# Performance work log

Measured on AMD Instinct MI355X. Metric: run time of the kernel, lower is better.

## Reference

```python
import jax, jax.numpy as jnp
import numpy as np

N, M, P = 4096, 4096, 32


def setup_inputs() -> dict:
    key = jax.random.key(0)
    k1, k2 = jax.random.split(key)
    x1 = jax.random.normal(k1, (N, P), dtype=jnp.float32)
    x2 = jax.random.normal(k2, (M, P), dtype=jnp.float32)
    log_rho = jnp.zeros((), dtype=jnp.float32)    # log(1.0)
    log_sigma = jnp.zeros((), dtype=jnp.float32)  # log(1.0)
    return {"x1": x1, "x2": x2, "log_rho": log_rho, "log_sigma": log_sigma}


def reference(x1, x2, log_rho, log_sigma):
    # sigma = exp(log_sigma)^2, rho = exp(log_rho), as in the module's __call__
    sigma = jnp.square(jnp.exp(log_sigma))
    rho = jnp.exp(log_rho)
    xs = x1 / rho  # (n, p)
    ys = x2 / rho  # (m, p)
    # avoids the (n, m, p) broadcasted intermediate of the naive form
    xn = jnp.sum(jnp.square(xs), axis=-1)  # (n,)
    yn = jnp.sum(jnp.square(ys), axis=-1)  # (m,)
    d = xn[:, None] + yn[None, :] - 2.0 * jnp.einsum("np,mp->nm", xs, ys)
    d = jnp.maximum(d, 0.0)  # clamp tiny negative rounding
    K = sigma * jnp.exp(-0.5 * d)  # (n, m)
    return K
```

## Files before the change

### kernel.cpp

```cpp
#include <hip/hip_runtime.h>

#define NN 4096
#define MM 4096
#define PP 32
#define LDA 40

typedef short bf16x8 __attribute__((ext_vector_type(8)));
typedef float f32x4  __attribute__((ext_vector_type(4)));

__device__ __forceinline__ unsigned short f32_to_bf16_rtn(float f) {
    unsigned u = __float_as_uint(f);
    u += 0x7FFF + ((u >> 16) & 1);
    return (unsigned short)(u >> 16);
}

__launch_bounds__(256, 4)
__global__ void eq_fused_mfma_kernel(const float* __restrict__ x1,
                                     const float* __restrict__ x2,
                                     const float* __restrict__ log_rho,
                                     const float* __restrict__ log_sigma,
                                     float* __restrict__ out) {
    __shared__ unsigned short Ah[128 * LDA];
    __shared__ unsigned short Al[128 * LDA];
    __shared__ unsigned short Bh[128 * LDA];
    __shared__ unsigned short Bl[128 * LDA];

    const int t  = threadIdx.x;
    const int bx = blockIdx.x;
    const int by = blockIdx.y;

    {
        const int row  = t >> 1;
        const int half = t & 1;
        {
            const float* src = x1 + (size_t)(by * 128 + row) * PP + half * 16;
            float partial = 0.f;
#pragma unroll
            for (int g = 0; g < 2; ++g) {
                float4 a = *reinterpret_cast<const float4*>(src + g * 8);
                float4 b = *reinterpret_cast<const float4*>(src + g * 8 + 4);
                float vs[8] = {a.x, a.y, a.z, a.w, b.x, b.y, b.z, b.w};
                bf16x8 hv, lv;
#pragma unroll
                for (int e = 0; e < 8; ++e) {
                    float v = vs[e];
                    partial = fmaf(v, v, partial);
                    unsigned short h = f32_to_bf16_rtn(v);
                    hv[e] = (short)h;
                    lv[e] = (short)f32_to_bf16_rtn(v - __uint_as_float((unsigned)h << 16));
                }
                int off = row * LDA + half * 16 + g * 8;
                *reinterpret_cast<bf16x8*>(&Ah[off]) = hv;
                *reinterpret_cast<bf16x8*>(&Al[off]) = lv;
            }
            float full = partial + __shfl_xor(partial, 1);
            if (half == 0) *reinterpret_cast<float*>(&Ah[row * LDA + 32]) = full;
        }
        {
            const float* src = x2 + (size_t)(bx * 128 + row) * PP + half * 16;
            float partial = 0.f;
#pragma unroll
            for (int g = 0; g < 2; ++g) {
                float4 a = *reinterpret_cast<const float4*>(src + g * 8);
                float4 b = *reinterpret_cast<const float4*>(src + g * 8 + 4);
                float vs[8] = {a.x, a.y, a.z, a.w, b.x, b.y, b.z, b.w};
                bf16x8 hv, lv;
#pragma unroll
                for (int e = 0; e < 8; ++e) {
                    float v = vs[e];
                    partial = fmaf(v, v, partial);
                    unsigned short h = f32_to_bf16_rtn(v);
                    hv[e] = (short)h;
                    lv[e] = (short)f32_to_bf16_rtn(v - __uint_as_float((unsigned)h << 16));
                }
                int off = row * LDA + half * 16 + g * 8;
                *reinterpret_cast<bf16x8*>(&Bh[off]) = hv;
                *reinterpret_cast<bf16x8*>(&Bl[off]) = lv;
            }
            float full = partial + __shfl_xor(partial, 1);
            if (half == 0) *reinterpret_cast<float*>(&Bh[row * LDA + 32]) = full;
        }
    }

    const float inv_rho2 = __expf(-2.f * log_rho[0]);
    const float sigma    = __expf(2.f * log_sigma[0]);
    const float nh_ir2   = -0.5f * inv_rho2;

    __syncthreads();

    const int w    = t >> 6;
    const int l    = t & 63;
    const int lo16 = l & 15;
    const int kg   = l >> 4;

    bf16x8 ah[2], al[2];
    float xh[2];
#pragma unroll
    for (int s = 0; s < 2; ++s) {
        int r   = w * 32 + s * 16 + lo16;
        int off = r * LDA + kg * 8;
        ah[s] = *reinterpret_cast<const bf16x8*>(&Ah[off]);
        al[s] = *reinterpret_cast<const bf16x8*>(&Al[off]);
        xh[s] = nh_ir2 * *reinterpret_cast<const float*>(&Ah[r * LDA + 32]);
    }

    const int rbase = by * 128 + w * 32;
    const int cb0   = bx * 128;

#pragma unroll
    for (int ct = 0; ct < 8; ++ct) {
        int off = (ct * 16 + lo16) * LDA + kg * 8;
        bf16x8 bh = *reinterpret_cast<const bf16x8*>(&Bh[off]);
        bf16x8 bl = *reinterpret_cast<const bf16x8*>(&Bl[off]);
        float yh[4];
#pragma unroll
        for (int j = 0; j < 4; ++j)
            yh[j] = nh_ir2 * *reinterpret_cast<const float*>(&Bh[(ct * 16 + kg * 4 + j) * LDA + 32]);
        const int colbase = cb0 + ct * 16 + kg * 4;
#pragma unroll
        for (int s = 0; s < 2; ++s) {
            f32x4 acc = {0.f, 0.f, 0.f, 0.f};
            acc = __builtin_amdgcn_mfma_f32_16x16x32_bf16(bh, ah[s], acc, 0, 0, 0);
            acc = __builtin_amdgcn_mfma_f32_16x16x32_bf16(bh, al[s], acc, 0, 0, 0);
            acc = __builtin_amdgcn_mfma_f32_16x16x32_bf16(bl, ah[s], acc, 0, 0, 0);
            f32x4 K;
            float u0 = fminf(fmaf(inv_rho2, acc[0], xh[s] + yh[0]), 0.f);
            float u1 = fminf(fmaf(inv_rho2, acc[1], xh[s] + yh[1]), 0.f);
            float u2 = fminf(fmaf(inv_rho2, acc[2], xh[s] + yh[2]), 0.f);
            float u3 = fminf(fmaf(inv_rho2, acc[3], xh[s] + yh[3]), 0.f);
            K[0] = sigma * __expf(u0);
            K[1] = sigma * __expf(u1);
            K[2] = sigma * __expf(u2);
            K[3] = sigma * __expf(u3);
            const int row = rbase + s * 16 + lo16;
            *reinterpret_cast<f32x4*>(&out[(size_t)row * MM + colbase]) = K;
        }
    }
}

extern "C" void kernel_launch(void* const* d_in, const int* in_sizes, int n_in,
                              void* d_out, int out_size, void* d_ws, size_t ws_size,
                              hipStream_t stream) {
    const float* x1        = (const float*)d_in[0];
    const float* x2        = (const float*)d_in[1];
    const float* log_rho   = (const float*)d_in[2];
    const float* log_sigma = (const float*)d_in[3];
    float* out = (float*)d_out;

    dim3 grid(MM / 128, NN / 128);
    eq_fused_mfma_kernel<<<grid, 256, 0, stream>>>(x1, x2, log_rho, log_sigma, out);
}
```

Before: 19.60 us.

## Split B tile staging across barrier and fold sigma into exp2 argument

The x2 tile is now loaded into registers up front. Only the first 64 rows are written to LDS before the barrier; the remaining rows are written after it, and a second barrier separates the first four column tiles from the last four, so the early output stores overlap with finishing the B staging. The sigma multiply and exp are replaced by a single exp2 whose argument carries log2e and 2·log_sigma, with the clamp moved to ls2. This adds a second block-wide barrier and changes the numerical form of the exponent.

New measurement: 19.51 us. About the same (-0.4%).

```diff
diff --git a/kernel.cpp b/kernel.cpp
--- a/kernel.cpp
+++ b/kernel.cpp
@@ -7,6 +7,8 @@
 
 typedef short bf16x8 __attribute__((ext_vector_type(8)));
 typedef float f32x4  __attribute__((ext_vector_type(4)));
+
+#define LOG2E 1.44269504088896f
 
 __device__ __forceinline__ unsigned short f32_to_bf16_rtn(float f) {
     unsigned u = __float_as_uint(f);
@@ -29,64 +31,89 @@
     const int bx = blockIdx.x;
     const int by = blockIdx.y;
 
+    const int row  = t >> 1;
+    const int half = t & 1;
+
+    const float* srcB = x2 + (size_t)(bx * 128 + row) * PP + half * 16;
+    float4 bg[4];
+    bg[0] = *reinterpret_cast<const float4*>(srcB + 0);
+    bg[1] = *reinterpret_cast<const float4*>(srcB + 4);
+    bg[2] = *reinterpret_cast<const float4*>(srcB + 8);
+    bg[3] = *reinterpret_cast<const float4*>(srcB + 12);
+
     {
-        const int row  = t >> 1;
-        const int half = t & 1;
-        {
-            const float* src = x1 + (size_t)(by * 128 + row) * PP + half * 16;
-            float partial = 0.f;
+        const float* src = x1 + (size_t)(by * 128 + row) * PP + half * 16;
+        float partial = 0.f;
 #pragma unroll
-            for (int g = 0; g < 2; ++g) {
-                float4 a = *reinterpret_cast<const float4*>(src + g * 8);
-                float4 b = *reinterpret_cast<const float4*>(src + g * 8 + 4);
-                float vs[8] = {a.x, a.y, a.z, a.w, b.x, b.y, b.z, b.w};
-                bf16x8 hv, lv;
+        for (int g = 0; g < 2; ++g) {
+            float4 a = *reinterpret_cast<const float4*>(src + g * 8);
+            float4 b = *reinterpret_cast<const float4*>(src + g * 8 + 4);
+            float vs[8] = {a.x, a.y, a.z, a.w, b.x, b.y, b.z, b.w};
+            bf16x8 hv, lv;
 #pragma unroll
-                for (int e = 0; e < 8; ++e) {
-                    float v = vs[e];
-                    partial = fmaf(v, v, partial);
-                    unsigned short h = f32_to_bf16_rtn(v);
-                    hv[e] = (short)h;
-                    lv[e] = (short)f32_to_bf16_rtn(v - __uint_as_float((unsigned)h << 16));
-                }
-                int off = row * LDA + half * 16 + g * 8;
-                *reinterpret_cast<bf16x8*>(&Ah[off]) = hv;
-                *reinterpret_cast<bf16x8*>(&Al[off]) = lv;
+            for (int e = 0; e < 8; ++e) {
+                float v = vs[e];
+                partial = fmaf(v, v, partial);
+                unsigned short h = f32_to_bf16_rtn(v);
+                hv[e] = (short)h;
+                lv[e] = (short)f32_to_bf16_rtn(v - __uint_as_float((unsigned)h << 16));
             }
-            float full = partial + __shfl_xor(partial, 1);
-            if (half == 0) *reinterpret_cast<float*>(&Ah[row * LDA + 32]) = full;
+            int off = row * LDA + half * 16 + g * 8;
+            *reinterpret_cast<bf16x8*>(&Ah[off]) = hv;
+            *reinterpret_cast<bf16x8*>(&Al[off]) = lv;
         }
-        {
-            const float* src = x2 + (size_t)(bx * 128 + row) * PP + half * 16;
-            float partial = 0.f;
+        float full = partial + __shfl_xor(partial, 1);
+        if (half == 0) *reinterpret_cast<float*>(&Ah[row * LDA + 32]) = full;
+    }
+
+    bf16x8 bhv[2], blv[2];
+    float bfull;
+    {
+        float partial = 0.f;
 #pragma unroll
-            for (int g = 0; g < 2; ++g) {
-                float4 a = *reinterpret_cast<const float4*>(src + g * 8);
-                float4 b = *reinterpret_cast<const float4*>(src + g * 8 + 4);
-                float vs[8] = {a.x, a.y, a.z, a.w, b.x, b.y, b.z, b.w};
-                bf16x8 hv, lv;
+        for (int g = 0; g < 2; ++g) {
+            float vs[8] = {bg[2*g].x, bg[2*g].y, bg[2*g].z, bg[2*g].w,
+                           bg[2*g+1].x, bg[2*g+1].y, bg[2*g+1].z, bg[2*g+1].w};
+            bf16x8 hv, lv;
 #pragma unroll
-                for (int e = 0; e < 8; ++e) {
-                    float v = vs[e];
-                    partial = fmaf(v, v, partial);
-                    unsigned short h = f32_to_bf16_rtn(v);
-                    hv[e] = (short)h;
-                    lv[e] = (short)f32_to_bf16_rtn(v - __uint_as_float((unsigned)h << 16));
-                }
-                int off = row * LDA + half * 16 + g * 8;
-                *reinterpret_cast<bf16x8*>(&Bh[off]) = hv;
-                *reinterpret_cast<bf16x8*>(&Bl[off]) = lv;
+            for (int e = 0; e < 8; ++e) {
+                float v = vs[e];
+                partial = fmaf(v, v, partial);
+                unsigned short h = f32_to_bf16_rtn(v);
+                hv[e] = (short)h;
+                lv[e] = (short)f32_to_bf16_rtn(v - __uint_as_float((unsigned)h << 16));
             }
-            float full = partial + __shfl_xor(partial, 1);
-            if (half == 0) *reinterpret_cast<float*>(&Bh[row * LDA + 32]) = full;
+            bhv[g] = hv; blv[g] = lv;
         }
+        bfull = partial + __shfl_xor(partial, 1);
+    }
+
+    if (row < 64) {
+#pragma unroll
+        for (int g = 0; g < 2; ++g) {
+            int off = row * LDA + half * 16 + g * 8;
+            *reinterpret_cast<bf16x8*>(&Bh[off]) = bhv[g];
+            *reinterpret_cast<bf16x8*>(&Bl[off]) = blv[g];
+        }
+        if (half == 0) *reinterpret_cast<float*>(&Bh[row * LDA + 32]) = bfull;
     }
 
     const float inv_rho2 = __expf(-2.f * log_rho[0]);
-    const float sigma    = __expf(2.f * log_sigma[0]);
-    const float nh_ir2   = -0.5f * inv_rho2;
+    const float ir2l2    = inv_rho2 * LOG2E;
+    const float nh       = -0.5f * ir2l2;
+    const float ls2      = 2.f * LOG2E * log_sigma[0];
 
     __syncthreads();
+
+    if (row >= 64) {
+#pragma unroll
+        for (int g = 0; g < 2; ++g) {
+            int off = row * LDA + half * 16 + g * 8;
+            *reinterpret_cast<bf16x8*>(&Bh[off]) = bhv[g];
+            *reinterpret_cast<bf16x8*>(&Bl[off]) = blv[g];
+        }
+        if (half == 0) *reinterpret_cast<float*>(&Bh[row * LDA + 32]) = bfull;
+    }
 
     const int w    = t >> 6;
     const int l    = t & 63;
@@ -101,21 +128,20 @@
         int off = r * LDA + kg * 8;
         ah[s] = *reinterpret_cast<const bf16x8*>(&Ah[off]);
         al[s] = *reinterpret_cast<const bf16x8*>(&Al[off]);
-        xh[s] = nh_ir2 * *reinterpret_cast<const float*>(&Ah[r * LDA + 32]);
+        xh[s] = nh * *reinterpret_cast<const float*>(&Ah[r * LDA + 32]);
     }
 
     const int rbase = by * 128 + w * 32;
     const int cb0   = bx * 128;
 
-#pragma unroll
-    for (int ct = 0; ct < 8; ++ct) {
+    auto do_ct = [&](int ct) {
         int off = (ct * 16 + lo16) * LDA + kg * 8;
         bf16x8 bh = *reinterpret_cast<const bf16x8*>(&Bh[off]);
         bf16x8 bl = *reinterpret_cast<const bf16x8*>(&Bl[off]);
-        float yh[4];
+        float yb[4];
 #pragma unroll
         for (int j = 0; j < 4; ++j)
-            yh[j] = nh_ir2 * *reinterpret_cast<const float*>(&Bh[(ct * 16 + kg * 4 + j) * LDA + 32]);
+            yb[j] = fmaf(nh, *reinterpret_cast<const float*>(&Bh[(ct * 16 + kg * 4 + j) * LDA + 32]), ls2);
         const int colbase = cb0 + ct * 16 + kg * 4;
 #pragma unroll
         for (int s = 0; s < 2; ++s) {
@@ -124,18 +150,21 @@
             acc = __builtin_amdgcn_mfma_f32_16x16x32_bf16(bh, al[s], acc, 0, 0, 0);
             acc = __builtin_amdgcn_mfma_f32_16x16x32_bf16(bl, ah[s], acc, 0, 0, 0);
             f32x4 K;
-            float u0 = fminf(fmaf(inv_rho2, acc[0], xh[s] + yh[0]), 0.f);
-            float u1 = fminf(fmaf(inv_rho2, acc[1], xh[s] + yh[1]), 0.f);
-            float u2 = fminf(fmaf(inv_rho2, acc[2], xh[s] + yh[2]), 0.f);
-            float u3 = fminf(fmaf(inv_rho2, acc[3], xh[s] + yh[3]), 0.f);
-            K[0] = sigma * __expf(u0);
-            K[1] = sigma * __expf(u1);
-            K[2] = sigma * __expf(u2);
-            K[3] = sigma * __expf(u3);
-            const int row = rbase + s * 16 + lo16;
-            *reinterpret_cast<f32x4*>(&out[(size_t)row * MM + colbase]) = K;
+#pragma unroll
+            for (int r = 0; r < 4; ++r) {
+                float u = fmaf(ir2l2, acc[r], xh[s] + yb[r]);
+                K[r] = exp2f(fminf(u, ls2));
+            }
+            const int orow = rbase + s * 16 + lo16;
+            *reinterpret_cast<f32x4*>(&out[(size_t)orow * MM + colbase]) = K;
         }
-    }
+    };
+
+#pragma unroll
+    for (int ct = 0; ct < 4; ++ct) do_ct(ct);
+    __syncthreads();
+#pragma unroll
+    for (int ct = 4; ct < 8; ++ct) do_ct(ct);
 }
 
 extern "C" void kernel_launch(void* const* d_in, const int* in_sizes, int n_in,
```
